# Performance work log

Hardware: AMD Instinct MI355X
Metric: run time of the kernel (lower is better)

## Reference

```python
import jax, jax.numpy as jnp
import numpy as np

EPS = 1e-8

def setup_inputs() -> dict:
    key = jax.random.key(0)
    ks = jax.random.split(key, 10)
    N, IN, Z, C, H = 8192, 512, 128, 64, 50
    x = jax.random.normal(ks[0], (N, IN), dtype=jnp.float32)
    c = jax.random.randint(ks[1], (N, 1), 0, C, dtype=jnp.int64)
    z = jax.random.normal(ks[2], (N, Z), dtype=jnp.float32)
    # f_x MLP params (Linear(IN,50) -> ReLU -> Linear(50,Z))
    W1 = jax.random.normal(ks[3], (IN, H), dtype=jnp.float32) / np.sqrt(IN)
    b1 = jax.random.normal(ks[4], (H,), dtype=jnp.float32) * 0.01
    W2 = jax.random.normal(ks[5], (H, Z), dtype=jnp.float32) / np.sqrt(H)
    b2 = jax.random.normal(ks[6], (Z,), dtype=jnp.float32) * 0.01
    # f_z Linear(Z,Z)
    Wz = jax.random.normal(ks[7], (Z, Z), dtype=jnp.float32) / np.sqrt(Z)
    bz = jax.random.normal(ks[8], (Z,), dtype=jnp.float32) * 0.01
    # per-category bilinear weights w_s [C,Z,Z] (torch.randn init)
    Ws = jax.random.normal(ks[9], (C, Z, Z), dtype=jnp.float32)
    return {"x": x, "c": c, "z": z, "W1": W1, "b1": b1, "W2": W2, "b2": b2, "Wz": Wz, "bz": bz, "Ws": Ws}

def reference(x, c, z, W1, b1, W2, b2, Wz, bz, Ws):
    cf = c.reshape(-1)                                    # [N]
    fx = jax.nn.relu(x @ W1 + b1) @ W2 + b2               # [N,Z]
    fz = z @ Wz + bz                                      # [N,Z]
    # per-sample bilinear: u[n] = fx[n] @ Ws[c[n]]
    u = jnp.einsum('nd,nde->ne', fx, Ws[cf])              # [N,Z]
    T = jax.nn.softplus(jnp.einsum('ne,ne->n', u, fz))    # [N]
    # neg_T[i] = mean over j with c[j]==c[i] of softplus(fx[i] @ Ws[c[i]] @ fz[j])
    S = jax.nn.softplus(u @ fz.T)                         # [N,N]
    mask = (cf[:, None] == cf[None, :]).astype(S.dtype)   # [N,N]
    neg_T = (S * mask).sum(axis=1) / mask.sum(axis=1)     # [N]
    return jnp.log(T + EPS) - jnp.log(neg_T + EPS)
```

## Files before the change

kernel.cpp:

```cpp
#include <hip/hip_runtime.h>
#include <math.h>

#define N_   8192
#define IN_  512
#define ZD   128
#define CC   64
#define HD   50
#define EPSF 1e-8f

typedef float vf4 __attribute__((ext_vector_type(4)));
typedef __attribute__((ext_vector_type(8))) short bfrag;

#define MFMA16(a, b, c) __builtin_amdgcn_mfma_f32_16x16x32_bf16((a), (b), (c), 0, 0, 0)

__device__ __forceinline__ float softplus_f(float t) {
    return fmaxf(t, 0.f) + log1pf(expf(-fabsf(t)));
}
__device__ __forceinline__ unsigned short bf16_rn(float x) {
    unsigned int u = __float_as_uint(x);
    return (unsigned short)((u + 0x7fff + ((u >> 16) & 1)) >> 16);
}
__device__ __forceinline__ float bf16_f(unsigned short h) {
    return __uint_as_float(((unsigned int)h) << 16);
}

__global__ __launch_bounds__(256) void k_pre(const int* __restrict__ c,
                                             const float* __restrict__ W1,
                                             const float* __restrict__ z,
                                             const float* __restrict__ Wz,
                                             const float* __restrict__ bz,
                                             const float* __restrict__ Ws,
                                             float* __restrict__ W1t,
                                             float* __restrict__ fz,
                                             unsigned short* __restrict__ fz_hi,
                                             unsigned short* __restrict__ Wst_hi,
                                             unsigned short* __restrict__ Wst_lo,
                                             int* __restrict__ counts,
                                             int* __restrict__ offsets,
                                             int* __restrict__ grouped) {
    __shared__ float smem[64 * 129];
    int tid = threadIdx.x;
    int b   = blockIdx.x;
    if (b < CC) {
        __shared__ int hist[CC];
        __shared__ int cursor;
        __shared__ int off_s;
        if (tid < CC) hist[tid] = 0;
        if (tid == 0) cursor = 0;
        __syncthreads();
        for (int i = tid; i < N_; i += 256) atomicAdd(&hist[c[i]], 1);
        __syncthreads();
        if (tid == 0) {
            int off = 0;
            for (int q = 0; q < b; ++q) off += hist[q];
            off_s = off;
            counts[b]  = hist[b];
            offsets[b] = off;
        }
        __syncthreads();
        int off = off_s;
        for (int i = tid; i < N_; i += 256) {
            if (c[i] == b) {
                int p = atomicAdd(&cursor, 1);
                grouped[off + p] = i;
            }
        }
    } else if (b < 192) {
        int idx = (b - 64) * 256 + tid;
        int d = idx >> 6, k = idx & 63;
        float v = (k < HD) ? W1[d * HD + k] : 0.f;
        W1t[k * IN_ + d] = v;
    } else if (b < 448) {
        float* sz = smem;
        int row0 = (b - 192) * 32;
        vf4* s4 = (vf4*)sz;
        const vf4* z4 = (const vf4*)(z + (size_t)row0 * ZD);
        #pragma unroll
        for (int f = 0; f < 4; ++f) s4[tid + f * 256] = z4[tid + f * 256];
        __syncthreads();
        int cp = tid & 31, rg = tid >> 5;
        const vf4* Wz4 = (const vf4*)Wz;
        vf4 bb = ((const vf4*)bz)[cp];
        vf4 acc[4];
        #pragma unroll
        for (int r = 0; r < 4; ++r) acc[r] = bb;
        #pragma unroll 1
        for (int d4 = 0; d4 < 32; ++d4) {
            vf4 w0 = Wz4[(4 * d4 + 0) * 32 + cp];
            vf4 w1 = Wz4[(4 * d4 + 1) * 32 + cp];
            vf4 w2 = Wz4[(4 * d4 + 2) * 32 + cp];
            vf4 w3 = Wz4[(4 * d4 + 3) * 32 + cp];
            #pragma unroll
            for (int r = 0; r < 4; ++r) {
                vf4 a = s4[(rg * 4 + r) * 32 + d4];
                acc[r] += a[0] * w0;
                acc[r] += a[1] * w1;
                acc[r] += a[2] * w2;
                acc[r] += a[3] * w3;
            }
        }
        vf4* fz4 = (vf4*)fz;
        #pragma unroll
        for (int r = 0; r < 4; ++r) {
            int n = row0 + rg * 4 + r;
            fz4[(size_t)n * 32 + cp] = acc[r];
            ushort4 h;
            h.x = bf16_rn(acc[r][0]); h.y = bf16_rn(acc[r][1]);
            h.z = bf16_rn(acc[r][2]); h.w = bf16_rn(acc[r][3]);
            *(ushort4*)(fz_hi + (size_t)n * ZD + cp * 4) = h;
        }
    } else {
        int cat = b - 448;
        const float* Wc = Ws + (size_t)cat * ZD * ZD;
        unsigned short* Whi = Wst_hi + (size_t)cat * ZD * ZD;
        unsigned short* Wlo = Wst_lo + (size_t)cat * ZD * ZD;
        #pragma unroll 1
        for (int half = 0; half < 2; ++half) {
            __syncthreads();
            const vf4* src = (const vf4*)(Wc + (size_t)half * 64 * ZD);
            #pragma unroll
            for (int f = 0; f < 8; ++f) {
                int idx = tid + f * 256;
                int row = idx >> 5, q = idx & 31;
                vf4 v = src[idx];
                #pragma unroll
                for (int e = 0; e < 4; ++e) smem[row * 129 + q * 4 + e] = v[e];
            }
            __syncthreads();
            #pragma unroll 1
            for (int f = 0; f < 32; ++f) {
                int idx = tid + f * 256;
                int e = idx >> 6, dd = idx & 63;
                float v = smem[dd * 129 + e];
                unsigned short h = bf16_rn(v);
                Whi[(size_t)e * ZD + half * 64 + dd] = h;
                Wlo[(size_t)e * ZD + half * 64 + dd] = bf16_rn(v - bf16_f(h));
            }
        }
    }
}

#define PAD 17
__global__ __launch_bounds__(256) void k_hfx(const float* __restrict__ x,
                                             const float* __restrict__ W1t,
                                             const float* __restrict__ b1,
                                             const float* __restrict__ W2,
                                             const float* __restrict__ b2,
                                             unsigned short* __restrict__ fx_hi,
                                             unsigned short* __restrict__ fx_lo) {
    __shared__ float sx[32 * 4 * PAD];
    __shared__ float sw[64 * 4 * PAD];
    __shared__ float sh[32 * 4 * PAD];
    int tid  = threadIdx.x;
    int row0 = blockIdx.x * 32;
    vf4* sx4 = (vf4*)sx;
    vf4* sw4 = (vf4*)sw;
    const vf4* x4g  = (const vf4*)x;
    const vf4* W1t4 = (const vf4*)W1t;

    int cp = tid & 15, rg = tid >> 4;
    float acc0[4] = {0.f, 0.f, 0.f, 0.f};
    float acc1[4] = {0.f, 0.f, 0.f, 0.f};

    #pragma unroll 1
    for (int kc = 0; kc < 8; ++kc) {
        __syncthreads();
        #pragma unroll
        for (int f = 0; f < 2; ++f) {
            int idx = tid + f * 256;
            int row = idx >> 4, q = idx & 15;
            sx4[row * PAD + q] = x4g[(size_t)(row0 + row) * 128 + kc * 16 + q];
        }
        #pragma unroll
        for (int f = 0; f < 4; ++f) {
            int idx = tid + f * 256;
            int k = idx >> 4, q = idx & 15;
            sw4[k * PAD + q] = W1t4[(size_t)k * 128 + kc * 16 + q];
        }
        __syncthreads();
        #pragma unroll 2
        for (int d4 = 0; d4 < 16; ++d4) {
            vf4 a0 = sx4[(2 * rg + 0) * PAD + d4];
            vf4 a1 = sx4[(2 * rg + 1) * PAD + d4];
            #pragma unroll
            for (int i = 0; i < 4; ++i) {
                vf4 w = sw4[(cp + 16 * i) * PAD + d4];
                acc0[i] += a0[0] * w[0] + a0[1] * w[1] + a0[2] * w[2] + a0[3] * w[3];
                acc1[i] += a1[0] * w[0] + a1[1] * w[1] + a1[2] * w[2] + a1[3] * w[3];
            }
        }
    }
    __syncthreads();
    #pragma unroll
    for (int i = 0; i < 4; ++i) {
        int k = cp + 16 * i;
        float bb = (k < HD) ? b1[k] : 0.f;
        sh[(2 * rg + 0) * 4 * PAD + k] = fmaxf(acc0[i] + bb, 0.f);
        sh[(2 * rg + 1) * 4 * PAD + k] = fmaxf(acc1[i] + bb, 0.f);
    }
    __syncthreads();
    {
        int cp2 = tid & 31, rg2 = tid >> 5;
        const vf4* W24 = (const vf4*)W2;
        const vf4* sh4 = (const vf4*)sh;
        vf4 bb = ((const vf4*)b2)[cp2];
        vf4 acc[4];
        #pragma unroll
        for (int r = 0; r < 4; ++r) acc[r] = bb;
        #pragma unroll 1
        for (int d4 = 0; d4 < 12; ++d4) {
            vf4 w0 = W24[(4 * d4 + 0) * 32 + cp2];
            vf4 w1 = W24[(4 * d4 + 1) * 32 + cp2];
            vf4 w2 = W24[(4 * d4 + 2) * 32 + cp2];
            vf4 w3 = W24[(4 * d4 + 3) * 32 + cp2];
            #pragma unroll
            for (int r = 0; r < 4; ++r) {
                vf4 a = sh4[(rg2 * 4 + r) * PAD + d4];
                acc[r] += a[0] * w0;
                acc[r] += a[1] * w1;
                acc[r] += a[2] * w2;
                acc[r] += a[3] * w3;
            }
        }
        #pragma unroll 1
        for (int d = 48; d < HD; ++d) {
            vf4 w = W24[d * 32 + cp2];
            #pragma unroll
            for (int r = 0; r < 4; ++r)
                acc[r] += sh[(rg2 * 4 + r) * 4 * PAD + d] * w;
        }
        #pragma unroll
        for (int r = 0; r < 4; ++r) {
            size_t n = (size_t)(row0 + rg2 * 4 + r);
            ushort4 h, l;
            #pragma unroll
            for (int e = 0; e < 4; ++e) {
                unsigned short hh = bf16_rn(acc[r][e]);
                ((unsigned short*)&h)[e] = hh;
                ((unsigned short*)&l)[e] = bf16_rn(acc[r][e] - bf16_f(hh));
            }
            *(ushort4*)(fx_hi + n * ZD + cp2 * 4) = h;
            *(ushort4*)(fx_lo + n * ZD + cp2 * 4) = l;
        }
    }
}

#define TI 4
__global__ __launch_bounds__(256) void k_fused(const unsigned short* __restrict__ fx_hi,
                                               const unsigned short* __restrict__ fx_lo,
                                               const unsigned short* __restrict__ Wst_hi,
                                               const unsigned short* __restrict__ Wst_lo,
                                               const float* __restrict__ fz,
                                               const unsigned short* __restrict__ fz_hi,
                                               const int* __restrict__ grouped,
                                               const int* __restrict__ offsets,
                                               const int* __restrict__ counts,
                                               float* __restrict__ out) {
    __shared__ uint4 sWhi[128 * 17];
    __shared__ uint4 sWlo[128 * 17];
    int tid = threadIdx.x;
    int cat = blockIdx.x >> 2;
    int t   = blockIdx.x & (TI - 1);
    int off = offsets[cat], cnt = counts[cat];
    int i0 = t * 64;
    if (i0 >= cnt) return;
    int mI = min(64, cnt - i0);

    int lane = tid & 63, wave = tid >> 6;
    int m = lane & 15, quad = lane >> 4;

    const uint4* gh = (const uint4*)(Wst_hi + (size_t)cat * ZD * ZD);
    const uint4* gl = (const uint4*)(Wst_lo + (size_t)cat * ZD * ZD);
    #pragma unroll
    for (int f = 0; f < 8; ++f) {
        int idx = tid + f * 256;
        int e = idx >> 4, q = idx & 15;
        sWhi[e * 17 + q] = gh[idx];
        sWlo[e * 17 + q] = gl[idx];
    }

    int irow = wave * 16 + m;
    int n_gA = grouped[off + i0 + min(irow, mI - 1)];
    const unsigned short* fhp = fx_hi + (size_t)n_gA * ZD + quad * 8;
    const unsigned short* flp = fx_lo + (size_t)n_gA * ZD + quad * 8;
    bfrag a_hi[4], a_lo[4];
    #pragma unroll
    for (int kb = 0; kb < 4; ++kb) {
        a_hi[kb] = *(const bfrag*)(fhp + kb * 32);
        a_lo[kb] = *(const bfrag*)(flp + kb * 32);
    }
    __syncthreads();

    vf4 uacc[8];
    #pragma unroll 1
    for (int et = 0; et < 8; ++et) {
        vf4 acc = {0.f, 0.f, 0.f, 0.f};
        #pragma unroll
        for (int kb = 0; kb < 4; ++kb) {
            bfrag bh = *(const bfrag*)&sWhi[(et * 16 + m) * 17 + kb * 4 + quad];
            bfrag bl = *(const bfrag*)&sWlo[(et * 16 + m) * 17 + kb * 4 + quad];
            acc = MFMA16(a_hi[kb], bh, acc);
            acc = MFMA16(a_hi[kb], bl, acc);
            acc = MFMA16(a_lo[kb], bh, acc);
        }
        uacc[et] = acc;
    }

    int nrow[4];
    float p[4] = {0.f, 0.f, 0.f, 0.f};
    #pragma unroll
    for (int r = 0; r < 4; ++r) {
        int ir = wave * 16 + quad * 4 + r;
        nrow[r] = (ir < mI) ? grouped[off + i0 + ir] : -1;
    }
    #pragma unroll 1
    for (int et = 0; et < 8; ++et) {
        #pragma unroll
        for (int r = 0; r < 4; ++r) {
            if (nrow[r] >= 0)
                p[r] += uacc[et][r] * fz[(size_t)nrow[r] * ZD + et * 16 + m];
        }
    }
    #pragma unroll
    for (int r = 0; r < 4; ++r) {
        float v = p[r];
        #pragma unroll
        for (int s = 8; s >= 1; s >>= 1) v += __shfl_xor(v, s, 64);
        p[r] = v;
    }
    float logT_r[4];
    #pragma unroll
    for (int r = 0; r < 4; ++r) logT_r[r] = logf(softplus_f(p[r]) + EPSF);

    __syncthreads();
    unsigned short* su = (unsigned short*)sWhi;
    #pragma unroll
    for (int et = 0; et < 8; ++et) {
        #pragma unroll
        for (int r = 0; r < 4; ++r) {
            int row = wave * 16 + quad * 4 + r;
            su[row * 136 + et * 16 + m] = bf16_rn(uacc[et][r]);
        }
    }
    __syncthreads();

    bfrag na[4];
    #pragma unroll
    for (int kb = 0; kb < 4; ++kb)
        na[kb] = *(const bfrag*)&su[(wave * 16 + m) * 136 + kb * 32 + quad * 8];

    uint4* sB = (uint4*)sWlo;
    float negsum[4] = {0.f, 0.f, 0.f, 0.f};

    #pragma unroll 1
    for (int jb = 0; jb < cnt; jb += 64) {
        int mJ = min(64, cnt - jb);
        __syncthreads();
        #pragma unroll
        for (int f = 0; f < 4; ++f) {
            int idx = tid + f * 256;
            int jr = idx >> 4, q = idx & 15;
            uint4 v = {0u, 0u, 0u, 0u};
            if (jr < mJ) {
                int j_g = grouped[off + jb + jr];
                v = *(const uint4*)(fz_hi + (size_t)j_g * ZD + q * 8);
            }
            sB[jr * 17 + q] = v;
        }
        __syncthreads();
        #pragma unroll 1
        for (int jt = 0; jt < 4; ++jt) {
            vf4 acc = {0.f, 0.f, 0.f, 0.f};
            #pragma unroll
            for (int kb = 0; kb < 4; ++kb) {
                bfrag b = *(const bfrag*)&sB[(jt * 16 + m) * 17 + kb * 4 + quad];
                acc = MFMA16(na[kb], b, acc);
            }
            bool jok = (jt * 16 + m) < mJ;
            #pragma unroll
            for (int r = 0; r < 4; ++r)
                if (jok) negsum[r] += softplus_f(acc[r]);
        }
    }

    #pragma unroll
    for (int r = 0; r < 4; ++r) {
        float v = negsum[r];
        #pragma unroll
        for (int s = 8; s >= 1; s >>= 1) v += __shfl_xor(v, s, 64);
        negsum[r] = v;
    }
    if (m == 0) {
        #pragma unroll
        for (int r = 0; r < 4; ++r) {
            if (nrow[r] >= 0)
                out[nrow[r]] = logT_r[r] - logf(negsum[r] / (float)cnt + EPSF);
        }
    }
}

extern "C" void kernel_launch(void* const* d_in, const int* in_sizes, int n_in,
                              void* d_out, int out_size, void* d_ws, size_t ws_size,
                              hipStream_t stream) {
    const float* x  = (const float*)d_in[0];
    const int*   c  = (const int*)  d_in[1];
    const float* z  = (const float*)d_in[2];
    const float* W1 = (const float*)d_in[3];
    const float* b1 = (const float*)d_in[4];
    const float* W2 = (const float*)d_in[5];
    const float* b2 = (const float*)d_in[6];
    const float* Wz = (const float*)d_in[7];
    const float* bz = (const float*)d_in[8];
    const float* Ws = (const float*)d_in[9];
    float* out = (float*)d_out;

    float* ws = (float*)d_ws;
    float* W1t = ws;
    float* fz  = W1t + 64 * IN_;
    unsigned short* fx_hi  = (unsigned short*)(fz + (size_t)N_ * ZD);
    unsigned short* fx_lo  = fx_hi + (size_t)N_ * ZD;
    unsigned short* fz_hi  = fx_lo + (size_t)N_ * ZD;
    unsigned short* Wst_hi = fz_hi + (size_t)N_ * ZD;
    unsigned short* Wst_lo = Wst_hi + (size_t)CC * ZD * ZD;
    int* counts  = (int*)(Wst_lo + (size_t)CC * ZD * ZD);
    int* offsets = counts + CC;
    int* grouped = offsets + CC;

    k_pre   <<<512, 256, 0, stream>>>(c, W1, z, Wz, bz, Ws, W1t, fz, fz_hi,
                                      Wst_hi, Wst_lo, counts, offsets, grouped);
    k_hfx   <<<N_ / 32, 256, 0, stream>>>(x, W1t, b1, W2, b2, fx_hi, fx_lo);
    k_fused <<<CC * TI, 256, 0, stream>>>(fx_hi, fx_lo, Wst_hi, Wst_lo, fz,
                                          fz_hi, grouped, offsets, counts, out);
}
```

Baseline: 158.0 us.

## Move f_x MLP to bf16x3 MFMA with pre-packed weight fragments

Rewrites the f_x MLP kernel (x@W1, ReLU, @W2) to use bf16 MFMA with a hi/lo split (three MFMAs per product) in place of scalar FP32 FMA loops. The preprocessing kernel now packs W1 and W2 into MFMA-fragment layout as hi/lo bf16 pairs, replacing the plain W1 transpose. Each block now handles 64 rows, x is read straight from global memory into registers, and the packed weights are staged in LDS. This is meant to cut the FP32 compute cost of the first GEMM, at the price of split-bf16 accuracy and more LDS use per block.

Measured after the change: 147.9 us (median of 2 runs). -6.3%, faster.

```diff
diff --git a/kernel.cpp b/kernel.cpp
--- a/kernel.cpp
+++ b/kernel.cpp
@@ -23,14 +23,24 @@
 __device__ __forceinline__ float bf16_f(unsigned short h) {
     return __uint_as_float(((unsigned int)h) << 16);
 }
+__device__ __forceinline__ void split8(const float* v, bfrag& hi, bfrag& lo) {
+    #pragma unroll
+    for (int e = 0; e < 8; ++e) {
+        unsigned short h = bf16_rn(v[e]);
+        ((short*)&hi)[e] = (short)h;
+        ((short*)&lo)[e] = (short)bf16_rn(v[e] - bf16_f(h));
+    }
+}
 
 __global__ __launch_bounds__(256) void k_pre(const int* __restrict__ c,
                                              const float* __restrict__ W1,
                                              const float* __restrict__ z,
                                              const float* __restrict__ Wz,
                                              const float* __restrict__ bz,
+                                             const float* __restrict__ W2,
                                              const float* __restrict__ Ws,
-                                             float* __restrict__ W1t,
+                                             uint4* __restrict__ W1p,
+                                             uint4* __restrict__ W2p,
                                              float* __restrict__ fz,
                                              unsigned short* __restrict__ fz_hi,
                                              unsigned short* __restrict__ Wst_hi,
@@ -65,14 +75,43 @@
                 grouped[off + p] = i;
             }
         }
-    } else if (b < 192) {
-        int idx = (b - 64) * 256 + tid;
-        int d = idx >> 6, k = idx & 63;
-        float v = (k < HD) ? W1[d * HD + k] : 0.f;
-        W1t[k * IN_ + d] = v;
-    } else if (b < 448) {
+    } else if (b < 80) {
+        int unit = (b - 64) * 256 + tid;
+        int lane = unit & 63, f = (unit >> 6) & 15, kc = unit >> 10;
+        int nt = f >> 2, ks = f & 3;
+        int n = nt * 16 + (lane & 15);
+        int kbase = kc * 128 + ks * 32 + (lane >> 4) * 8;
+        unsigned short hi8[8], lo8[8];
+        #pragma unroll
+        for (int j = 0; j < 8; ++j) {
+            int k = kbase + j;
+            float v = (n < HD) ? W1[k * HD + n] : 0.f;
+            unsigned short h = bf16_rn(v);
+            hi8[j] = h;
+            lo8[j] = bf16_rn(v - bf16_f(h));
+        }
+        W1p[kc * 2048 + f * 64 + lane]        = *(uint4*)hi8;
+        W1p[kc * 2048 + 1024 + f * 64 + lane] = *(uint4*)lo8;
+    } else if (b < 84) {
+        int unit = (b - 80) * 256 + tid;
+        int lane = unit & 63, f = unit >> 6;
+        int nt = f >> 1, ks = f & 1;
+        int n = nt * 16 + (lane & 15);
+        int kbase = ks * 32 + (lane >> 4) * 8;
+        unsigned short hi8[8], lo8[8];
+        #pragma unroll
+        for (int j = 0; j < 8; ++j) {
+            int k = kbase + j;
+            float v = (k < HD) ? W2[k * ZD + n] : 0.f;
+            unsigned short h = bf16_rn(v);
+            hi8[j] = h;
+            lo8[j] = bf16_rn(v - bf16_f(h));
+        }
+        W2p[f * 64 + lane]        = *(uint4*)hi8;
+        W2p[1024 + f * 64 + lane] = *(uint4*)lo8;
+    } else if (b < 340) {
         float* sz = smem;
-        int row0 = (b - 192) * 32;
+        int row0 = (b - 84) * 32;
         vf4* s4 = (vf4*)sz;
         const vf4* z4 = (const vf4*)(z + (size_t)row0 * ZD);
         #pragma unroll
@@ -110,7 +149,7 @@
             *(ushort4*)(fz_hi + (size_t)n * ZD + cp * 4) = h;
         }
     } else {
-        int cat = b - 448;
+        int cat = b - 340;
         const float* Wc = Ws + (size_t)cat * ZD * ZD;
         unsigned short* Whi = Wst_hi + (size_t)cat * ZD * ZD;
         unsigned short* Wlo = Wst_lo + (size_t)cat * ZD * ZD;
@@ -140,107 +179,92 @@
     }
 }
 
-#define PAD 17
 __global__ __launch_bounds__(256) void k_hfx(const float* __restrict__ x,
-                                             const float* __restrict__ W1t,
+                                             const uint4* __restrict__ W1p,
+                                             const uint4* __restrict__ W2p,
                                              const float* __restrict__ b1,
-                                             const float* __restrict__ W2,
                                              const float* __restrict__ b2,
                                              unsigned short* __restrict__ fx_hi,
                                              unsigned short* __restrict__ fx_lo) {
-    __shared__ float sx[32 * 4 * PAD];
-    __shared__ float sw[64 * 4 * PAD];
-    __shared__ float sh[32 * 4 * PAD];
-    int tid  = threadIdx.x;
-    int row0 = blockIdx.x * 32;
-    vf4* sx4 = (vf4*)sx;
-    vf4* sw4 = (vf4*)sw;
-    const vf4* x4g  = (const vf4*)x;
-    const vf4* W1t4 = (const vf4*)W1t;
-
-    int cp = tid & 15, rg = tid >> 4;
-    float acc0[4] = {0.f, 0.f, 0.f, 0.f};
-    float acc1[4] = {0.f, 0.f, 0.f, 0.f};
+    __shared__ uint4 sW2[2048];
+    __shared__ uint4 sW1[2048];
+    __shared__ float sh[64 * 68];
+    int tid = threadIdx.x;
+    int lane = tid & 63, w = tid >> 6, m = lane & 15, quad = lane >> 4;
+    int i0 = blockIdx.x * 64;
+
+    #pragma unroll
+    for (int f = 0; f < 8; ++f) sW2[tid + f * 256] = W2p[tid + f * 256];
+
+    int row = i0 + w * 16 + m;
+    const float4* xr = (const float4*)(x + (size_t)row * IN_);
+
+    vf4 acc[4];
+    #pragma unroll
+    for (int nt = 0; nt < 4; ++nt) acc[nt] = (vf4){0.f, 0.f, 0.f, 0.f};
 
     #pragma unroll 1
-    for (int kc = 0; kc < 8; ++kc) {
-        __syncthreads();
-        #pragma unroll
-        for (int f = 0; f < 2; ++f) {
-            int idx = tid + f * 256;
-            int row = idx >> 4, q = idx & 15;
-            sx4[row * PAD + q] = x4g[(size_t)(row0 + row) * 128 + kc * 16 + q];
-        }
-        #pragma unroll
-        for (int f = 0; f < 4; ++f) {
-            int idx = tid + f * 256;
-            int k = idx >> 4, q = idx & 15;
-            sw4[k * PAD + q] = W1t4[(size_t)k * 128 + kc * 16 + q];
-        }
-        __syncthreads();
-        #pragma unroll 2
-        for (int d4 = 0; d4 < 16; ++d4) {
-            vf4 a0 = sx4[(2 * rg + 0) * PAD + d4];
-            vf4 a1 = sx4[(2 * rg + 1) * PAD + d4];
+    for (int kc = 0; kc < 4; ++kc) {
+        __syncthreads();
+        #pragma unroll
+        for (int f = 0; f < 8; ++f)
+            sW1[tid + f * 256] = W1p[kc * 2048 + tid + f * 256];
+        __syncthreads();
+        #pragma unroll 1
+        for (int ks = 0; ks < 4; ++ks) {
+            float4 xa = xr[kc * 32 + ks * 8 + quad * 2];
+            float4 xb = xr[kc * 32 + ks * 8 + quad * 2 + 1];
+            float xv[8] = {xa.x, xa.y, xa.z, xa.w, xb.x, xb.y, xb.z, xb.w};
+            bfrag ah, al;
+            split8(xv, ah, al);
             #pragma unroll
-            for (int i = 0; i < 4; ++i) {
-                vf4 w = sw4[(cp + 16 * i) * PAD + d4];
-                acc0[i] += a0[0] * w[0] + a0[1] * w[1] + a0[2] * w[2] + a0[3] * w[3];
-                acc1[i] += a1[0] * w[0] + a1[1] * w[1] + a1[2] * w[2] + a1[3] * w[3];
-            }
-        }
+            for (int nt = 0; nt < 4; ++nt) {
+                bfrag bh = *(const bfrag*)&sW1[(nt * 4 + ks) * 64 + lane];
+                bfrag bl = *(const bfrag*)&sW1[1024 + (nt * 4 + ks) * 64 + lane];
+                acc[nt] = MFMA16(ah, bh, acc[nt]);
+                acc[nt] = MFMA16(ah, bl, acc[nt]);
+                acc[nt] = MFMA16(al, bh, acc[nt]);
+            }
+        }
+    }
+    #pragma unroll
+    for (int nt = 0; nt < 4; ++nt) {
+        int col = nt * 16 + m;
+        float bb = (col < HD) ? b1[col] : 0.f;
+        #pragma unroll
+        for (int r = 0; r < 4; ++r)
+            sh[(w * 16 + quad * 4 + r) * 68 + col] = fmaxf(acc[nt][r] + bb, 0.f);
     }
     __syncthreads();
-    #pragma unroll
-    for (int i = 0; i < 4; ++i) {
-        int k = cp + 16 * i;
-        float bb = (k < HD) ? b1[k] : 0.f;
-        sh[(2 * rg + 0) * 4 * PAD + k] = fmaxf(acc0[i] + bb, 0.f);
-        sh[(2 * rg + 1) * 4 * PAD + k] = fmaxf(acc1[i] + bb, 0.f);
-    }
-    __syncthreads();
-    {
-        int cp2 = tid & 31, rg2 = tid >> 5;
-        const vf4* W24 = (const vf4*)W2;
-        const vf4* sh4 = (const vf4*)sh;
-        vf4 bb = ((const vf4*)b2)[cp2];
-        vf4 acc[4];
-        #pragma unroll
-        for (int r = 0; r < 4; ++r) acc[r] = bb;
-        #pragma unroll 1
-        for (int d4 = 0; d4 < 12; ++d4) {
-            vf4 w0 = W24[(4 * d4 + 0) * 32 + cp2];
-            vf4 w1 = W24[(4 * d4 + 1) * 32 + cp2];
-            vf4 w2 = W24[(4 * d4 + 2) * 32 + cp2];
-            vf4 w3 = W24[(4 * d4 + 3) * 32 + cp2];
-            #pragma unroll
-            for (int r = 0; r < 4; ++r) {
-                vf4 a = sh4[(rg2 * 4 + r) * PAD + d4];
-                acc[r] += a[0] * w0;
-                acc[r] += a[1] * w1;
-                acc[r] += a[2] * w2;
-                acc[r] += a[3] * w3;
-            }
-        }
-        #pragma unroll 1
-        for (int d = 48; d < HD; ++d) {
-            vf4 w = W24[d * 32 + cp2];
-            #pragma unroll
-            for (int r = 0; r < 4; ++r)
-                acc[r] += sh[(rg2 * 4 + r) * 4 * PAD + d] * w;
-        }
+
+    bfrag ah2[2], al2[2];
+    #pragma unroll
+    for (int ks = 0; ks < 2; ++ks) {
+        const float4* shp = (const float4*)&sh[(w * 16 + m) * 68 + ks * 32 + quad * 8];
+        float4 ha = shp[0], hb = shp[1];
+        float hv[8] = {ha.x, ha.y, ha.z, ha.w, hb.x, hb.y, hb.z, hb.w};
+        split8(hv, ah2[ks], al2[ks]);
+    }
+    #pragma unroll 1
+    for (int nt = 0; nt < 8; ++nt) {
+        vf4 a2 = {0.f, 0.f, 0.f, 0.f};
+        #pragma unroll
+        for (int ks = 0; ks < 2; ++ks) {
+            bfrag bh = *(const bfrag*)&sW2[(nt * 2 + ks) * 64 + lane];
+            bfrag bl = *(const bfrag*)&sW2[1024 + (nt * 2 + ks) * 64 + lane];
+            a2 = MFMA16(ah2[ks], bh, a2);
+            a2 = MFMA16(ah2[ks], bl, a2);
+            a2 = MFMA16(al2[ks], bh, a2);
+        }
+        int col = nt * 16 + m;
+        float bb2 = b2[col];
         #pragma unroll
         for (int r = 0; r < 4; ++r) {
-            size_t n = (size_t)(row0 + rg2 * 4 + r);
-            ushort4 h, l;
-            #pragma unroll
-            for (int e = 0; e < 4; ++e) {
-                unsigned short hh = bf16_rn(acc[r][e]);
-                ((unsigned short*)&h)[e] = hh;
-                ((unsigned short*)&l)[e] = bf16_rn(acc[r][e] - bf16_f(hh));
-            }
-            *(ushort4*)(fx_hi + n * ZD + cp2 * 4) = h;
-            *(ushort4*)(fx_lo + n * ZD + cp2 * 4) = l;
+            size_t rg = (size_t)(i0 + w * 16 + quad * 4 + r);
+            float v = a2[r] + bb2;
+            unsigned short hh = bf16_rn(v);
+            fx_hi[rg * ZD + col] = hh;
+            fx_lo[rg * ZD + col] = bf16_rn(v - bf16_f(hh));
         }
     }
 }
@@ -338,8 +362,8 @@
     for (int et = 0; et < 8; ++et) {
         #pragma unroll
         for (int r = 0; r < 4; ++r) {
-            int row = wave * 16 + quad * 4 + r;
-            su[row * 136 + et * 16 + m] = bf16_rn(uacc[et][r]);
+            int rowq = wave * 16 + quad * 4 + r;
+            su[rowq * 136 + et * 16 + m] = bf16_rn(uacc[et][r]);
         }
     }
     __syncthreads();
@@ -373,8 +397,8 @@
             vf4 acc = {0.f, 0.f, 0.f, 0.f};
             #pragma unroll
             for (int kb = 0; kb < 4; ++kb) {
-                bfrag b = *(const bfrag*)&sB[(jt * 16 + m) * 17 + kb * 4 + quad];
-                acc = MFMA16(na[kb], b, acc);
+                bfrag bb = *(const bfrag*)&sB[(jt * 16 + m) * 17 + kb * 4 + quad];
+                acc = MFMA16(na[kb], bb, acc);
             }
             bool jok = (jt * 16 + m) < mJ;
             #pragma unroll
@@ -414,9 +438,9 @@
     const float* Ws = (const float*)d_in[9];
     float* out = (float*)d_out;
 
-    float* ws = (float*)d_ws;
-    float* W1t = ws;
-    float* fz  = W1t + 64 * IN_;
+    uint4* W1p = (uint4*)d_ws;
+    uint4* W2p = W1p + 8192;
+    float* fz  = (float*)(W2p + 2048);
     unsigned short* fx_hi  = (unsigned short*)(fz + (size_t)N_ * ZD);
     unsigned short* fx_lo  = fx_hi + (size_t)N_ * ZD;
     unsigned short* fz_hi  = fx_lo + (size_t)N_ * ZD;
@@ -426,9 +450,10 @@
     int* offsets = counts + CC;
     int* grouped = offsets + CC;
 
-    k_pre   <<<512, 256, 0, stream>>>(c, W1, z, Wz, bz, Ws, W1t, fz, fz_hi,
-                                      Wst_hi, Wst_lo, counts, offsets, grouped);
-    k_hfx   <<<N_ / 32, 256, 0, stream>>>(x, W1t, b1, W2, b2, fx_hi, fx_lo);
+    k_pre   <<<404, 256, 0, stream>>>(c, W1, z, Wz, bz, W2, Ws, W1p, W2p, fz,
+                                      fz_hi, Wst_hi, Wst_lo, counts, offsets,
+                                      grouped);
+    k_hfx   <<<N_ / 64, 256, 0, stream>>>(x, W1p, W2p, b1, b2, fx_hi, fx_lo);
     k_fused <<<CC * TI, 256, 0, stream>>>(fx_hi, fx_lo, Wst_hi, Wst_lo, fz,
                                           fz_hi, grouped, offsets, counts, out);
 }
```
